# Kernel optimization log

Hardware: AMD Instinct MI355X
Metric: run time of the kernel (lower is better)

## Reference

```python
import jax, jax.numpy as jnp
import numpy as np

B, T, D, H, L = 64, 256, 1024, 1024, 2


def setup_inputs() -> dict:
    key = jax.random.key(0)
    ks = jax.random.split(key, 14)
    s = 1.0 / np.sqrt(H)
    x = jax.random.normal(ks[0], (B, T, D), jnp.float32)
    lengths = jax.random.randint(ks[1], (B,), 1, T + 1)

    def u(k, shape):
        return jax.random.uniform(k, shape, jnp.float32, -s, s)

    # stacked per-layer weights; layer 0 input dim == H so stacking is valid
    fw_Wx = u(ks[2], (L, D, 4 * H))
    fw_Wh = u(ks[3], (L, H, 4 * H))
    fw_b = u(ks[4], (L, 4 * H))  # x2h.bias + h2h.bias folded into one
    bw_Wx = u(ks[5], (L, D, 4 * H))
    bw_Wh = u(ks[6], (L, H, 4 * H))
    bw_b = u(ks[7], (L, 4 * H))
    return dict(x=x, lengths=lengths, fw_Wx=fw_Wx, fw_Wh=fw_Wh, fw_b=fw_b,
                bw_Wx=bw_Wx, bw_Wh=bw_Wh, bw_b=bw_b)


def _run_direction(xs, valid, Wx, Wh, b):
    # xs: [T, B, D] in processing order; valid: [T, B, 1] mask by step index
    n_layers = Wx.shape[0]
    inp = xs
    hT = None
    for l in range(n_layers):
        Wx_l, Wh_l, b_l = Wx[l], Wh[l], b[l]

        def step(carry, sv, Wx_l=Wx_l, Wh_l=Wh_l, b_l=b_l):
            h, c = carry
            x_t, v = sv
            gates = x_t @ Wx_l + h @ Wh_l + b_l  # [B, 4H]
            i, f, g, o = jnp.split(gates, 4, axis=-1)
            c_new = jax.nn.sigmoid(f) * c + jax.nn.sigmoid(i) * jnp.tanh(g)
            h_new = jax.nn.sigmoid(o) * jnp.tanh(c_new)
            h2 = v * h_new + (1.0 - v) * h  # length masking: hold state past length
            c2 = v * c_new + (1.0 - v) * c
            return (h2, c2), h2

        z = jnp.zeros((xs.shape[1], Wh_l.shape[0]), xs.dtype)
        (hT, _), inp = jax.lax.scan(step, (z, z), (inp, valid))
    return inp, hT  # [T, B, H] (processing order), [B, H]


def reference(x, lengths, fw_Wx, fw_Wh, fw_b, bw_Wx, bw_Wh, bw_b):
    xs = jnp.transpose(x, (1, 0, 2))  # [T, B, D]
    # valid[s, b] = lengths[b] > s, indexed by step count (same for both dirs)
    valid = (lengths[None, :] > jnp.arange(T)[:, None]).astype(x.dtype)[:, :, None]
    fw_out, fw_last = _run_direction(xs, valid, fw_Wx, fw_Wh, fw_b)
    bw_out_rev, bw_last = _run_direction(xs[::-1], valid, bw_Wx, bw_Wh, bw_b)
    bw_out = bw_out_rev[::-1]  # back to original time order
    outputs = jnp.transpose(jnp.concatenate([fw_out, bw_out], -1), (1, 0, 2))  # [B, T, 2H]
    final = jnp.concatenate([fw_last, bw_last], -1)  # [B, 2H]
    return outputs, final
```

## Files before the change

kernel.cpp:

```cpp
#include <hip/hip_runtime.h>

#define NB 64
#define NT 256
#define ND 1024
#define NH 1024
#define G4 4096

typedef _Float16 half_t;
typedef half_t v8h __attribute__((ext_vector_type(8)));
typedef half_t h4  __attribute__((ext_vector_type(4)));
typedef float  v4f __attribute__((ext_vector_type(4)));

#define XPLANE ((size_t)NB * NT * ND)
#define HPLANE ((size_t)NB * NH)
#define WREG   16384

__global__ void cvt_x(const float* __restrict__ x, half_t* __restrict__ xh) {
    const int row = blockIdx.x;
    const int b = row >> 8, t = row & 255;
    const int o = threadIdx.x * 4;
    const float4 v = *(const float4*)(x + (size_t)row * ND + o);
    const size_t d = ((size_t)t * NB + b) * ND + o;
    h4 hh;
    hh.x = (half_t)v.x; hh.y = (half_t)v.y;
    hh.z = (half_t)v.z; hh.w = (half_t)v.w;
    *(h4*)(xh + d) = hh;
}

__global__ void transpose_pack(const float* __restrict__ fw_Wx,
                               const float* __restrict__ fw_Wh,
                               const float* __restrict__ bw_Wx,
                               const float* __restrict__ bw_Wh,
                               half_t* __restrict__ WT) {
    const int z = blockIdx.z;
    const int combo = z >> 1;
    const int half  = z & 1;
    const int layer = combo >> 1, dirb = combo & 1;
    const float* src = half ? (dirb ? bw_Wh : fw_Wh) : (dirb ? bw_Wx : fw_Wx);
    src += (size_t)layer * ND * G4;
    const int n0 = blockIdx.x * 64, k0 = blockIdx.y * 64;
    __shared__ float tile[64][65];
    const int t = threadIdx.x;
    #pragma unroll
    for (int it = 0; it < 4; ++it) {
        const int kr = it * 16 + (t >> 4);
        const int nc = (t & 15) * 4;
        const float4 v = *(const float4*)(src + (size_t)(k0 + kr) * G4 + n0 + nc);
        tile[kr][nc + 0] = v.x; tile[kr][nc + 1] = v.y;
        tile[kr][nc + 2] = v.z; tile[kr][nc + 3] = v.w;
    }
    __syncthreads();
    #pragma unroll
    for (int it = 0; it < 4; ++it) {
        const int nr = it * 16 + (t >> 4);
        const int kc = (t & 15) * 4;
        h4 hv;
        hv.x = (half_t)tile[kc + 0][nr];
        hv.y = (half_t)tile[kc + 1][nr];
        hv.z = (half_t)tile[kc + 2][nr];
        hv.w = (half_t)tile[kc + 3][nr];
        const int n = n0 + nr;
        const int kr1 = k0 + kc;
        const int gt = n >> 10, j = n & 1023;
        const int jp = j >> 4, l15j = j & 15;
        const int ki = kr1 >> 5, g2 = (kr1 >> 3) & 3, e0 = kr1 & 7;
        const int lane2 = g2 * 16 + l15j;
        const size_t r = (((size_t)combo * 64 + jp) * 4 + gt) * 2 + half;
        *(h4*)(WT + r * WREG + (size_t)ki * 512 + lane2 * 8 + e0) = hv;
    }
}

__device__ __forceinline__ void store_h2(half_t* p, half_t a, half_t b) {
    union { half_t h[2]; unsigned int u; } v;
    v.h[0] = a; v.h[1] = b;
    __hip_atomic_store((unsigned int*)p, v.u,
                       __ATOMIC_RELAXED, __HIP_MEMORY_SCOPE_AGENT);
}

__global__ __launch_bounds__(512, 2) void lstm_persistent(
        const half_t* __restrict__ xh,
        const int* __restrict__ lengths,
        const float* __restrict__ fw_b, const float* __restrict__ bw_b,
        const half_t* __restrict__ WT,
        half_t* __restrict__ hring,
        float* __restrict__ out,
        int* __restrict__ bar) {
    const int bid = blockIdx.x;
    const int c  = (bid & 7) >> 1;
    const int jp = ((bid >> 3) << 1) | (bid & 1);
    const int layer = c >> 1, dir = c & 1;
    const int tid = threadIdx.x;
    const int wv = tid >> 6, lane = tid & 63;
    const int gt = wv & 3, kh = wv >> 2;
    const int l15 = lane & 15, g = lane >> 4;
    const int j0 = jp * 16;

    const int shf  = tid >> 8;
    const int srow = (tid & 255) >> 2;
    const int sks  = (tid & 3) * 32;
    const int sswz = (srow & 7) << 3;
    const int rswz = (l15 & 7) << 3;

    __shared__ half_t alds[2][2][64][128];
    __shared__ float glds[4][2][NB][17];
    __shared__ float c_lds[NB][17];
    __shared__ float h_lds[NB][17];
    __shared__ float bias_lds[4][16];
    __shared__ int   len_lds[NB];

    for (int e = tid; e < NB * 16; e += 512) {
        c_lds[e >> 4][e & 15] = 0.f;
        h_lds[e >> 4][e & 15] = 0.f;
    }
    if (tid < NB) len_lds[tid] = lengths[tid];
    if (tid < 64) {
        const int gg = tid >> 4, jj = tid & 15;
        const float* bs = dir ? bw_b : fw_b;
        bias_lds[gg][jj] = bs[(size_t)layer * G4 + gg * NH + j0 + jj];
    }

    v8h w[32];
    {
        const half_t* wp = WT + ((((size_t)c * 64 + jp) * 4 + gt) * 2 + kh) * WREG
                         + (size_t)lane * 8;
        #pragma unroll
        for (int ki = 0; ki < 32; ++ki) w[ki] = *(const v8h*)(wp + (size_t)ki * 512);
    }
    #pragma unroll
    for (int ki = 0; ki < 32; ++ki) asm volatile("" : "+a"(w[ki]));
    __syncthreads();

    const int id128 = layer * 64 + jp;
    int* gcnt = bar + ((size_t)dir * 8 + (id128 >> 4)) * 16;
    int* root = bar + 256 + dir * 16;
    int* rel  = bar + 320 + dir * 16;

    for (int s = 0; s <= NT; ++s) {
        const bool active = (layer == 0) ? (s < NT) : (s >= 1);
        const int u = (layer == 0) ? s : (s - 1);

        const half_t* bsrc = nullptr;
        if (active) {
            if (shf == 0) {
                if (layer == 0) {
                    const int t = dir ? (NT - 1 - u) : u;
                    bsrc = xh + (size_t)t * NB * ND;
                } else {
                    bsrc = hring + ((size_t)s * 4 + dir) * HPLANE;
                }
            } else {
                bsrc = hring + ((size_t)u * 4 + c) * HPLANE;
            }
        }

        v4f acc[4];
        #pragma unroll
        for (int m = 0; m < 4; ++m) acc[m] = (v4f){0.f, 0.f, 0.f, 0.f};

        v8h sh[4];
        if (active) {
            const size_t o0 = (size_t)srow * 1024 + sks;
            #pragma unroll
            for (int i = 0; i < 4; ++i) sh[i] = *(const v8h*)(bsrc + o0 + i * 8);
        }

        #pragma unroll
        for (int ci = 0; ci < 8; ++ci) {
            if (active) {
                #pragma unroll
                for (int i = 0; i < 4; ++i)
                    *(v8h*)&alds[ci & 1][shf][srow][(sks + i * 8) ^ sswz] = sh[i];
                if (ci < 7) {
                    const size_t o = (size_t)srow * 1024 + (ci + 1) * 128 + sks;
                    #pragma unroll
                    for (int i = 0; i < 4; ++i) sh[i] = *(const v8h*)(bsrc + o + i * 8);
                }
            }
            __syncthreads();
            if (active) {
                #pragma unroll
                for (int ki = 0; ki < 4; ++ki) {
                    #pragma unroll
                    for (int m = 0; m < 4; ++m) {
                        v8h ah = *(const v8h*)&alds[ci & 1][kh][m * 16 + l15]
                                              [(ki * 32 + g * 8) ^ rswz];
                        acc[m] = __builtin_amdgcn_mfma_f32_16x16x32_f16(
                                     ah, w[ci * 4 + ki], acc[m], 0, 0, 0);
                    }
                }
            }
        }

        if (active) {
            #pragma unroll
            for (int m = 0; m < 4; ++m)
                #pragma unroll
                for (int r = 0; r < 4; ++r)
                    glds[gt][kh][m * 16 + g * 4 + r][l15] = acc[m][r];
        }
        __syncthreads();

        if (active) {
            const int b = tid >> 3, jj0 = (tid & 7) * 2;
            float hpair[2];
            #pragma unroll
            for (int k2 = 0; k2 < 2; ++k2) {
                const int jj = jj0 + k2;
                const float iv = glds[0][0][b][jj] + glds[0][1][b][jj] + bias_lds[0][jj];
                const float fv = glds[1][0][b][jj] + glds[1][1][b][jj] + bias_lds[1][jj];
                const float gv = glds[2][0][b][jj] + glds[2][1][b][jj] + bias_lds[2][jj];
                const float ov = glds[3][0][b][jj] + glds[3][1][b][jj] + bias_lds[3][jj];
                const float cold = c_lds[b][jj];
                const float hold = h_lds[b][jj];
                const float si = 1.f / (1.f + expf(-iv));
                const float sf = 1.f / (1.f + expf(-fv));
                const float so = 1.f / (1.f + expf(-ov));
                const float cn = sf * cold + si * tanhf(gv);
                const float hn = so * tanhf(cn);
                const bool valid = len_lds[b] > u;
                const float c2 = valid ? cn : cold;
                const float h2 = valid ? hn : hold;
                c_lds[b][jj] = c2;
                h_lds[b][jj] = h2;
                hpair[k2] = h2;
                if (layer == 1) {
                    const int tout = dir ? (NT - 1 - u) : u;
                    __builtin_nontemporal_store(
                        h2, &out[((size_t)b * NT + tout) * (2 * NH) + dir * NH + j0 + jj]);
                    if (u == NT - 1)
                        __builtin_nontemporal_store(
                            h2, &out[(size_t)NB * NT * (2 * NH) + (size_t)b * (2 * NH)
                                     + dir * NH + j0 + jj]);
                }
            }
            half_t* hb2 = hring + ((size_t)(u + 1) * 4 + c) * HPLANE
                        + (size_t)b * NH + j0 + jj0;
            store_h2(hb2, (half_t)hpair[0], (half_t)hpair[1]);
        }

        const int phase = s + 1;
        __syncthreads();
        if (tid == 0) {
            const int a = __hip_atomic_fetch_add(gcnt, 1, __ATOMIC_RELAXED,
                                                 __HIP_MEMORY_SCOPE_AGENT) + 1;
            if (a == phase * 16) {
                const int rr = __hip_atomic_fetch_add(root, 1, __ATOMIC_RELAXED,
                                                      __HIP_MEMORY_SCOPE_AGENT) + 1;
                if (rr == phase * 8)
                    __hip_atomic_store(rel, phase, __ATOMIC_RELAXED,
                                       __HIP_MEMORY_SCOPE_AGENT);
            }
            while (__hip_atomic_load(rel, __ATOMIC_RELAXED,
                                     __HIP_MEMORY_SCOPE_AGENT) < phase)
                __builtin_amdgcn_s_sleep(1);
        }
        __syncthreads();
    }
}

extern "C" void kernel_launch(void* const* d_in, const int* in_sizes, int n_in,
                              void* d_out, int out_size, void* d_ws, size_t ws_size,
                              hipStream_t stream) {
    (void)in_sizes; (void)n_in; (void)out_size; (void)ws_size;
    const float* x     = (const float*)d_in[0];
    const int*   len   = (const int*)d_in[1];
    const float* fw_Wx = (const float*)d_in[2];
    const float* fw_Wh = (const float*)d_in[3];
    const float* fw_b  = (const float*)d_in[4];
    const float* bw_Wx = (const float*)d_in[5];
    const float* bw_Wh = (const float*)d_in[6];
    const float* bw_b  = (const float*)d_in[7];
    float* out = (float*)d_out;

    char* ws = (char*)d_ws;
    size_t off = 0;
    half_t* WT = (half_t*)(ws + off); off += (size_t)2048 * WREG * 2;
    half_t* xh = (half_t*)(ws + off); off += XPLANE * 2;
    int* bar = (int*)(ws + off); off += 4096;
    half_t* hring = (half_t*)(ws + off);

    hipMemsetAsync(bar, 0, 4096 + (size_t)4 * HPLANE * 2, stream);

    cvt_x<<<NB * NT, 256, 0, stream>>>(x, xh);

    dim3 tg(G4 / 64, ND / 64, 8);
    transpose_pack<<<tg, 256, 0, stream>>>(fw_Wx, fw_Wh, bw_Wx, bw_Wh, WT);

    void* args[] = {(void*)&xh, (void*)&len, (void*)&fw_b, (void*)&bw_b,
                    (void*)&WT, (void*)&hring, (void*)&out, (void*)&bar};
    hipLaunchCooperativeKernel((void*)lstm_persistent, dim3(256), dim3(512),
                               args, 0, stream);
}
```

Measured before the change: 2.464 ms.

## Double K-chunk size, reduce gate partials via LDS atomics, use fast activations

Staging chunks grow from 128 to 256 columns, which halves the number of per-step chunk iterations and their barriers. The two K-half partial gate sums are now combined with LDS atomicAdd into a single bias-initialised buffer, replacing the separate per-half buffers and the explicit sum. Sigmoid and tanh switch to __expf/__fdividef fast approximations. In exchange, each thread holds more staging registers, LDS atomics can contend, the fast math costs some accuracy, and the glds bias initialisation is not separated by a barrier from the previous step's reads.

```diff
diff --git a/kernel.cpp b/kernel.cpp
--- a/kernel.cpp
+++ b/kernel.cpp
@@ -77,6 +77,13 @@
                        __ATOMIC_RELAXED, __HIP_MEMORY_SCOPE_AGENT);
 }
 
+__device__ __forceinline__ float fsig(float x) {
+    return __fdividef(1.f, 1.f + __expf(-x));
+}
+__device__ __forceinline__ float ftanh(float x) {
+    return 1.f - __fdividef(2.f, 1.f + __expf(2.f * x));
+}
+
 __global__ __launch_bounds__(512, 2) void lstm_persistent(
         const half_t* __restrict__ xh,
         const int* __restrict__ lengths,
@@ -97,12 +104,12 @@
 
     const int shf  = tid >> 8;
     const int srow = (tid & 255) >> 2;
-    const int sks  = (tid & 3) * 32;
+    const int sks  = (tid & 3) * 64;
     const int sswz = (srow & 7) << 3;
     const int rswz = (l15 & 7) << 3;
 
-    __shared__ half_t alds[2][2][64][128];
-    __shared__ float glds[4][2][NB][17];
+    __shared__ half_t alds[2][2][64][256];
+    __shared__ float glds[4][NB][17];
     __shared__ float c_lds[NB][17];
     __shared__ float h_lds[NB][17];
     __shared__ float bias_lds[4][16];
@@ -153,39 +160,46 @@
             }
         }
 
+        if (active) {
+            for (int e = tid; e < 4 * NB * 16; e += 512) {
+                const int gg = e >> 10, rem = e & 1023;
+                glds[gg][rem >> 4][rem & 15] = bias_lds[gg][rem & 15];
+            }
+        }
+
         v4f acc[4];
         #pragma unroll
         for (int m = 0; m < 4; ++m) acc[m] = (v4f){0.f, 0.f, 0.f, 0.f};
 
-        v8h sh[4];
+        v8h sh[8];
         if (active) {
             const size_t o0 = (size_t)srow * 1024 + sks;
             #pragma unroll
-            for (int i = 0; i < 4; ++i) sh[i] = *(const v8h*)(bsrc + o0 + i * 8);
+            for (int i = 0; i < 8; ++i) sh[i] = *(const v8h*)(bsrc + o0 + i * 8);
         }
 
         #pragma unroll
-        for (int ci = 0; ci < 8; ++ci) {
+        for (int ci = 0; ci < 4; ++ci) {
             if (active) {
                 #pragma unroll
-                for (int i = 0; i < 4; ++i)
+                for (int i = 0; i < 8; ++i)
                     *(v8h*)&alds[ci & 1][shf][srow][(sks + i * 8) ^ sswz] = sh[i];
-                if (ci < 7) {
-                    const size_t o = (size_t)srow * 1024 + (ci + 1) * 128 + sks;
+                if (ci < 3) {
+                    const size_t o = (size_t)srow * 1024 + (ci + 1) * 256 + sks;
                     #pragma unroll
-                    for (int i = 0; i < 4; ++i) sh[i] = *(const v8h*)(bsrc + o + i * 8);
+                    for (int i = 0; i < 8; ++i) sh[i] = *(const v8h*)(bsrc + o + i * 8);
                 }
             }
             __syncthreads();
             if (active) {
                 #pragma unroll
-                for (int ki = 0; ki < 4; ++ki) {
+                for (int ki = 0; ki < 8; ++ki) {
                     #pragma unroll
                     for (int m = 0; m < 4; ++m) {
                         v8h ah = *(const v8h*)&alds[ci & 1][kh][m * 16 + l15]
                                               [(ki * 32 + g * 8) ^ rswz];
                         acc[m] = __builtin_amdgcn_mfma_f32_16x16x32_f16(
-                                     ah, w[ci * 4 + ki], acc[m], 0, 0, 0);
+                                     ah, w[ci * 8 + ki], acc[m], 0, 0, 0);
                     }
                 }
             }
@@ -196,7 +210,7 @@
             for (int m = 0; m < 4; ++m)
                 #pragma unroll
                 for (int r = 0; r < 4; ++r)
-                    glds[gt][kh][m * 16 + g * 4 + r][l15] = acc[m][r];
+                    atomicAdd(&glds[gt][m * 16 + g * 4 + r][l15], acc[m][r]);
         }
         __syncthreads();
 
@@ -206,17 +220,17 @@
             #pragma unroll
             for (int k2 = 0; k2 < 2; ++k2) {
                 const int jj = jj0 + k2;
-                const float iv = glds[0][0][b][jj] + glds[0][1][b][jj] + bias_lds[0][jj];
-                const float fv = glds[1][0][b][jj] + glds[1][1][b][jj] + bias_lds[1][jj];
-                const float gv = glds[2][0][b][jj] + glds[2][1][b][jj] + bias_lds[2][jj];
-                const float ov = glds[3][0][b][jj] + glds[3][1][b][jj] + bias_lds[3][jj];
+                const float iv = glds[0][b][jj];
+                const float fv = glds[1][b][jj];
+                const float gv = glds[2][b][jj];
+                const float ov = glds[3][b][jj];
                 const float cold = c_lds[b][jj];
                 const float hold = h_lds[b][jj];
-                const float si = 1.f / (1.f + expf(-iv));
-                const float sf = 1.f / (1.f + expf(-fv));
-                const float so = 1.f / (1.f + expf(-ov));
-                const float cn = sf * cold + si * tanhf(gv);
-                const float hn = so * tanhf(cn);
+                const float si = fsig(iv);
+                const float sf = fsig(fv);
+                const float so = fsig(ov);
+                const float cn = sf * cold + si * ftanh(gv);
+                const float hn = so * ftanh(cn);
                 const bool valid = len_lds[b] > u;
                 const float c2 = valid ? cn : cold;
                 const float h2 = valid ? hn : hold;
```

After: 5.948 ms. 2.41x slower.
